# Kernel optimization log

Measured on AMD Instinct MI355X. Metric: run time of the kernel, lower is better.

The kernel has to match this reference:

```python
import jax, jax.numpy as jnp
import numpy as np

N_HEADS = 4
SIGMA = 1.0


def setup_inputs() -> dict:
    key = jax.random.key(0)
    k1, k2, k3, k4, k5 = jax.random.split(key, 5)
    B, T, N, C_IN, C_OUT, K1 = 2, 12, 10000, 64, 32, 17
    x = jax.random.normal(k1, (B, T, N, C_IN), dtype=jnp.float32)
    W = jax.random.normal(k2, (C_OUT, C_IN), dtype=jnp.float32) * (1.0 / np.sqrt(C_IN))
    b = jax.random.normal(k3, (C_OUT,), dtype=jnp.float32) * 0.01
    nearest_dist = jax.random.uniform(k4, (N, K1), dtype=jnp.float32)
    nearest_nodes = jax.random.randint(k5, (N, K1), 0, N, dtype=jnp.int32)
    return {"x": x, "W": W, "b": b, "nearest_dist": nearest_dist, "nearest_nodes": nearest_nodes}


def reference(x, W, b, nearest_dist, nearest_nodes):
    # Linear projection: (B,T,N,C_in) -> (B,T,N,C_out)
    x = jnp.einsum('btni,oi->btno', x, W) + b
    B, T, N, C = x.shape
    K1 = nearest_nodes.shape[1]  # k+1
    H = N_HEADS
    # pad row of zeros at index N (also reachable via index -1, matching torch)
    pad_x = jnp.concatenate([x, jnp.zeros_like(x[:, :, :1])], axis=2)  # (B,T,N+1,C)
    lam = jnp.arange(1, H + 1, dtype=x.dtype) / H  # (H,)
    nn_flat = nearest_nodes.reshape(-1)            # (N*K1,)
    d_flat = nearest_dist.reshape(-1)              # (N*K1,)
    w = jnp.exp(-(d_flat[:, None] ** 2) * lam / (SIGMA ** 2))  # (N*K1, H)
    w = jnp.where(nn_flat[:, None] == -1, 0.0, w)
    w = jnp.where(w < 1e-5, 0.0, w)
    # gather neighbor features and reduce over neighbor axis per head
    gathered = pad_x[:, :, nn_flat].reshape(B, T, N, K1, C)  # (B,T,N,K1,C)
    wk = w.reshape(N, K1, H)
    agg = jnp.einsum('btnkc,nkh->btnhc', gathered, wk)       # (B,T,N,H,C)
    d_clean = jnp.where(jnp.isinf(d_flat), 0.0, d_flat)
    dist_agg = (w * d_clean[:, None]).reshape(N, K1, H).sum(axis=1)  # (N,H)
    return agg + dist_agg[None, None, :, :, None]
```

## Files before the change

### kernel.cpp

```cpp
#include <hip/hip_runtime.h>
#include <hip/hip_bf16.h>
#include <math.h>

#define CIN   64
#define COUT  32
#define K1V   17
#define HV    4
#define BTILE 3

typedef float v4f __attribute__((ext_vector_type(4)));
typedef unsigned int v4u __attribute__((ext_vector_type(4)));
typedef short bf8s __attribute__((ext_vector_type(8)));
typedef float f32x16 __attribute__((ext_vector_type(16)));
typedef unsigned short u16;

__device__ __forceinline__ float bf2f(u16 h) {
  unsigned u = ((unsigned)h) << 16;
  return __builtin_bit_cast(float, u);
}
__device__ __forceinline__ unsigned cvt2(float lo, float hi) {
  __hip_bfloat162 p = __float22bfloat162_rn(make_float2(lo, hi));
  unsigned u;
  __builtin_memcpy(&u, &p, 4);
  return u;
}
__device__ __forceinline__ bf8s pack8(v4f a, v4f b) {
  v4u u = { cvt2(a.x, a.y), cvt2(a.z, a.w), cvt2(b.x, b.y), cvt2(b.z, b.w) };
  return __builtin_bit_cast(bf8s, u);
}
__device__ __forceinline__ u16 f2bf(float f) {
  __hip_bfloat16 h = __float2bfloat16(f);
  u16 u;
  __builtin_memcpy(&u, &h, 2);
  return u;
}

__global__ __launch_bounds__(256, 4) void proj_kernel(
    const float* __restrict__ x, const float* __restrict__ W,
    const float* __restrict__ b, u16* __restrict__ xp, long nrows, int N) {
  int tid = threadIdx.x;
  int wv  = tid >> 6;
  int l   = tid & 63;
  int lr  = l & 31;
  int lh  = l >> 5;
  long rbase = (long)blockIdx.x * 128 + wv * 32;
  if (rbase + lr >= nrows) return;

  const float* xr = x + (rbase + lr) * CIN + lh * 8;
  const float* wr = W + (long)lr * CIN + lh * 8;

  bf8s afr[4], bfr[4];
#pragma unroll
  for (int ks = 0; ks < 4; ++ks) {
    v4f xa = *(const v4f*)(xr + ks * 16);
    v4f xb = *(const v4f*)(xr + ks * 16 + 4);
    v4f wa = *(const v4f*)(wr + ks * 16);
    v4f wb = *(const v4f*)(wr + ks * 16 + 4);
    afr[ks] = pack8(xa, xb);
    bfr[ks] = pack8(wa, wb);
  }

  f32x16 acc;
#pragma unroll
  for (int i = 0; i < 16; ++i) acc[i] = 0.0f;
#pragma unroll
  for (int ks = 0; ks < 4; ++ks)
    acc = __builtin_amdgcn_mfma_f32_32x32x16_bf16(afr[ks], bfr[ks], acc, 0, 0, 0);

  float bias = b[lr];
  int bt0  = (int)(rbase / N);
  int rem0 = (int)(rbase - (long)bt0 * N);
#pragma unroll
  for (int r = 0; r < 16; ++r) {
    int rr = (r & 3) + 8 * (r >> 2) + 4 * lh;
    int n  = rem0 + rr;
    int bt = bt0;
    if (n >= N) { n -= N; bt += 1; }
    int j  = (bt * 21846) >> 16;
    int t  = bt - 3 * j;
    size_t off = ((size_t)((long)j * N + n) * 3 + t) * 32 + lr;
    xp[off] = f2bf(acc[r] + bias);
  }
}

__global__ __launch_bounds__(256) void gcn_kernel(
    const u16*   __restrict__ xp,
    const float* __restrict__ dist,
    const int*   __restrict__ nn,
    float* __restrict__ out,
    int N) {
  __shared__ float wl[8][K1V][HV];
  __shared__ float dl[8][K1V];
  __shared__ int   nl[8][K1V];
  __shared__ float dagl[8][HV];

  int tid = threadIdx.x;
  int jt  = blockIdx.y;
  int bt0 = jt * BTILE;
  int n0  = blockIdx.x * 8;

  if (tid < 8 * K1V) {
    int l = tid / K1V, k = tid % K1V;
    int n_ = n0 + l;
    float w0 = 0, w1 = 0, w2 = 0, w3 = 0, dc = 0;
    int idx = 0;
    if (n_ < N) {
      float d = dist[(long)n_ * K1V + k];
      idx = nn[(long)n_ * K1V + k];
      float d2 = d * d;
      w0 = __expf(-d2 * 0.25f);
      w1 = __expf(-d2 * 0.50f);
      w2 = __expf(-d2 * 0.75f);
      w3 = __expf(-d2);
      if (idx == -1) { w0 = w1 = w2 = w3 = 0.0f; }
      if (w0 < 1e-5f) w0 = 0.0f;
      if (w1 < 1e-5f) w1 = 0.0f;
      if (w2 < 1e-5f) w2 = 0.0f;
      if (w3 < 1e-5f) w3 = 0.0f;
      dc = isinf(d) ? 0.0f : d;
      if (idx < 0 || idx >= N) idx = 0;
    }
    wl[l][k][0] = w0; wl[l][k][1] = w1; wl[l][k][2] = w2; wl[l][k][3] = w3;
    dl[l][k] = dc; nl[l][k] = idx;
  }
  __syncthreads();

  if (tid < 8 * HV) {
    int l = tid >> 2, h = tid & 3;
    float s = 0.0f;
#pragma unroll
    for (int k = 0; k < K1V; ++k) s = fmaf(wl[l][k][h], dl[l][k], s);
    dagl[l][h] = s;
  }
  __syncthreads();

  int ln = tid >> 5;
  int c  = tid & 31;
  int n  = n0 + ln;
  if (n >= N) return;

  int off[K1V];
#pragma unroll
  for (int k = 0; k < K1V; ++k) off[k] = nl[ln][k] * (BTILE * COUT);

  const u16* base = xp + (size_t)jt * N * (BTILE * COUT) + c;

  float a[BTILE][HV];
#pragma unroll
  for (int t = 0; t < BTILE; ++t) {
    a[t][0] = dagl[ln][0]; a[t][1] = dagl[ln][1];
    a[t][2] = dagl[ln][2]; a[t][3] = dagl[ln][3];
  }

#pragma unroll
  for (int k = 0; k < K1V; ++k) {
    float v0 = bf2f(base[off[k]]);
    float v1 = bf2f(base[off[k] + COUT]);
    float v2 = bf2f(base[off[k] + 2 * COUT]);
    v4f w4 = *(const v4f*)&wl[ln][k][0];
    a[0][0] = fmaf(w4.x, v0, a[0][0]);
    a[0][1] = fmaf(w4.y, v0, a[0][1]);
    a[0][2] = fmaf(w4.z, v0, a[0][2]);
    a[0][3] = fmaf(w4.w, v0, a[0][3]);
    a[1][0] = fmaf(w4.x, v1, a[1][0]);
    a[1][1] = fmaf(w4.y, v1, a[1][1]);
    a[1][2] = fmaf(w4.z, v1, a[1][2]);
    a[1][3] = fmaf(w4.w, v1, a[1][3]);
    a[2][0] = fmaf(w4.x, v2, a[2][0]);
    a[2][1] = fmaf(w4.y, v2, a[2][1]);
    a[2][2] = fmaf(w4.z, v2, a[2][2]);
    a[2][3] = fmaf(w4.w, v2, a[2][3]);
  }

#pragma unroll
  for (int t = 0; t < BTILE; ++t) {
    float* ob = out + (((size_t)(bt0 + t) * N + n) * HV) * COUT + c;
    __builtin_nontemporal_store(a[t][0], ob);
    __builtin_nontemporal_store(a[t][1], ob + COUT);
    __builtin_nontemporal_store(a[t][2], ob + 2 * COUT);
    __builtin_nontemporal_store(a[t][3], ob + 3 * COUT);
  }
}

extern "C" void kernel_launch(void* const* d_in, const int* in_sizes, int n_in,
                              void* d_out, int out_size, void* d_ws, size_t ws_size,
                              hipStream_t stream) {
  const float* x    = (const float*)d_in[0];
  const float* W    = (const float*)d_in[1];
  const float* b    = (const float*)d_in[2];
  const float* dist = (const float*)d_in[3];
  const int*   nn   = (const int*)d_in[4];
  float* out = (float*)d_out;
  u16*   xp  = (u16*)d_ws;

  int  N  = in_sizes[4] / K1V;
  long M  = (long)in_sizes[0] / CIN;
  int  BT = (int)(M / N);

  proj_kernel<<<(int)((M + 127) / 128), 256, 0, stream>>>(x, W, b, xp, M, N);

  dim3 grid((N + 7) / 8, BT / BTILE);
  gcn_kernel<<<grid, 256, 0, stream>>>(xp, dist, nn, out, N);
}
```

Measured before the change: 61.55 us.

## Assign gcn work items per XCD via atomic counters for L2 locality

Each gcn block reads the hardware XCC id and claims a work item from a per-XCD atomic counter. Contiguous ranges of (time-tile, node-group) items therefore run on the same XCD, so that XCD's L2 can keep reusing that time slice of the projected features during the random neighbor gathers. In exchange it adds a memset launch, one atomic per block plus a block-wide sync, and a work-stealing fallback when an XCD's queue runs dry.

After: 67.20 us. +9.2%, slower.

```diff
diff --git a/kernel.cpp b/kernel.cpp
--- a/kernel.cpp
+++ b/kernel.cpp
@@ -7,6 +7,7 @@
 #define K1V   17
 #define HV    4
 #define BTILE 3
+#define NXCD  8
 
 typedef float v4f __attribute__((ext_vector_type(4)));
 typedef unsigned int v4u __attribute__((ext_vector_type(4)));
@@ -88,16 +89,35 @@
     const float* __restrict__ dist,
     const int*   __restrict__ nn,
     float* __restrict__ out,
-    int N) {
+    int*   __restrict__ ctr,
+    int N, int ngroups, int perq, int nitems) {
   __shared__ float wl[8][K1V][HV];
   __shared__ float dl[8][K1V];
   __shared__ int   nl[8][K1V];
   __shared__ float dagl[8][HV];
+  __shared__ int   s_item;
 
   int tid = threadIdx.x;
-  int jt  = blockIdx.y;
+  if (tid == 0) {
+    int xcc = __builtin_amdgcn_s_getreg(63508) & (NXCD - 1);
+    int item = -1;
+    for (int a = 0; a < NXCD; ++a) {
+      int q = (xcc + a) & (NXCD - 1);
+      int r = atomicAdd(&ctr[q * 16], 1);
+      if (r < perq) {
+        int cand = q * perq + r;
+        if (cand < nitems) { item = cand; break; }
+      }
+    }
+    s_item = item;
+  }
+  __syncthreads();
+  int item = s_item;
+  if (item < 0) return;
+
+  int jt  = item / ngroups;
+  int n0  = (item - jt * ngroups) * 8;
   int bt0 = jt * BTILE;
-  int n0  = blockIdx.x * 8;
 
   if (tid < 8 * K1V) {
     int l = tid / K1V, k = tid % K1V;
@@ -191,14 +211,22 @@
   const float* dist = (const float*)d_in[3];
   const int*   nn   = (const int*)d_in[4];
   float* out = (float*)d_out;
-  u16*   xp  = (u16*)d_ws;
+
+  int* ctr = (int*)d_ws;
+  u16* xp  = (u16*)((char*)d_ws + 512);
 
   int  N  = in_sizes[4] / K1V;
   long M  = (long)in_sizes[0] / CIN;
   int  BT = (int)(M / N);
 
+  hipMemsetAsync(ctr, 0, 512, stream);
+
   proj_kernel<<<(int)((M + 127) / 128), 256, 0, stream>>>(x, W, b, xp, M, N);
 
-  dim3 grid((N + 7) / 8, BT / BTILE);
-  gcn_kernel<<<grid, 256, 0, stream>>>(xp, dist, nn, out, N);
-}
+  int ngroups = (N + 7) / 8;
+  int njt     = BT / BTILE;
+  int nitems  = ngroups * njt;
+  int perq    = (nitems + NXCD - 1) / NXCD;
+  gcn_kernel<<<nitems, 256, 0, stream>>>(xp, dist, nn, out, ctr,
+                                         N, ngroups, perq, nitems);
+}
```
